# Kernel tuning notes

Hardware: AMD Instinct MI355X
Metric: run time of the kernel (lower is better)

Reference implementation:

```python
import jax, jax.numpy as jnp
import numpy as np

D_MODEL = 1024
N_HEADS = 16
D_FF = 4096
ROPE_THETA = 10000.0


def _rope(x, pos):
    # x: [B, H, S, D], pos: [S]
    D = x.shape[-1]
    inv_freq = ROPE_THETA ** (-jnp.arange(0, D, 2, dtype=jnp.float32) / D)  # [D/2]
    ang = pos.astype(jnp.float32)[:, None] * inv_freq[None, :]              # [S, D/2]
    cos, sin = jnp.cos(ang), jnp.sin(ang)
    x1, x2 = x[..., 0::2], x[..., 1::2]
    r1 = x1 * cos - x2 * sin
    r2 = x1 * sin + x2 * cos
    return jnp.stack([r1, r2], axis=-1).reshape(x.shape)


def _rmsnorm(x, g, eps=1e-5):
    xf = x.astype(jnp.float32)
    rms = jnp.sqrt(jnp.mean(xf * xf, axis=-1, keepdims=True) + eps)
    return (xf / rms * g).astype(x.dtype)


def _block(x, WQ, WK, WV, WO, W1, W2, W3, G1, G2):
    B, S, _ = x.shape
    H, Dh = N_HEADS, D_MODEL // N_HEADS
    pos = jnp.arange(S)

    h = _rmsnorm(x, G1)
    Q = (h @ WQ.T).reshape(B, S, H, Dh).transpose(0, 2, 1, 3)
    K = (h @ WK.T).reshape(B, S, H, Dh).transpose(0, 2, 1, 3)
    V = (h @ WV.T).reshape(B, S, H, Dh).transpose(0, 2, 1, 3)
    Q = _rope(Q, pos)
    K = _rope(K, pos)

    scores = jnp.einsum('bhqd,bhkd->bhqk', Q, K) / jnp.sqrt(jnp.float32(Dh))
    causal = jnp.triu(jnp.ones((S, S), dtype=bool), k=1)
    scores = jnp.where(causal, -jnp.inf, scores.astype(jnp.float32))
    probs = jax.nn.softmax(scores, axis=-1).astype(x.dtype)
    attn = jnp.einsum('bhqk,bhkd->bhqd', probs, V)
    attn = attn.transpose(0, 2, 1, 3).reshape(B, S, D_MODEL)
    x = x + attn @ WO.T

    h = _rmsnorm(x, G2)
    w1x = h @ W1.T
    w3x = h @ W3.T
    ffn = (w1x * jax.nn.sigmoid(w1x) * w3x) @ W2.T
    return x + ffn


def setup_inputs() -> dict:
    key = jax.random.key(0)
    ks = jax.random.split(key, 9)
    sig_a = np.sqrt(2.0 / (D_MODEL + D_MODEL))
    sig_f = np.sqrt(2.0 / (D_FF + D_MODEL))
    x = jax.random.normal(ks[0], (2, 2048, D_MODEL), dtype=jnp.float32)
    def tn(k, shape, sig):
        return jnp.clip(jax.random.normal(k, shape, dtype=jnp.float32) * sig, -3 * sig, 3 * sig)
    return {
        'x': x,
        'WQ': tn(ks[1], (D_MODEL, D_MODEL), sig_a),
        'WK': tn(ks[2], (D_MODEL, D_MODEL), sig_a),
        'WV': tn(ks[3], (D_MODEL, D_MODEL), sig_a),
        'WO': tn(ks[4], (D_MODEL, D_MODEL), sig_a),
        'W1': tn(ks[5], (D_FF, D_MODEL), sig_f),
        'W2': tn(ks[6], (D_MODEL, D_FF), sig_f),
        'W3': tn(ks[7], (D_FF, D_MODEL), sig_f),
        'G1': jnp.ones((D_MODEL,), dtype=jnp.float32),
        'G2': jnp.ones((D_MODEL,), dtype=jnp.float32),
    }


def reference(x, WQ, WK, WV, WO, W1, W2, W3, G1, G2):
    return _block(x, WQ, WK, WV, WO, W1, W2, W3, G1, G2)
```

## Files before the change

### kernel.cpp

```cpp
#include <hip/hip_runtime.h>
#include <stdint.h>

typedef __attribute__((ext_vector_type(8))) short bf16x8;
typedef __attribute__((ext_vector_type(4))) short short4v;
typedef __attribute__((ext_vector_type(4))) float f32x4;

#define MFMA16(a, b, c) __builtin_amdgcn_mfma_f32_16x16x32_bf16((a), (b), (c), 0, 0, 0)

__device__ __forceinline__ float b2f(short s) {
  unsigned u = ((unsigned)(unsigned short)s) << 16;
  return __builtin_bit_cast(float, u);
}
__device__ __forceinline__ short f2b(float f) {
  unsigned u = __builtin_bit_cast(unsigned, f);
  u = (u + 0x7fffu + ((u >> 16) & 1u)) >> 16;
  return (short)u;
}

__device__ __forceinline__ void gl_lds16(const short* g, short* l) {
  __builtin_amdgcn_global_load_lds((const __attribute__((address_space(1))) void*)g,
                                   (__attribute__((address_space(3))) void*)l, 16, 0, 0);
}

__global__ __launch_bounds__(256) void convert_kernel(const float* __restrict__ src,
                                                      short* __restrict__ dst, int n) {
  int i = (blockIdx.x * 256 + threadIdx.x) * 8;
  if (i >= n) return;
  f32x4 a = *(const f32x4*)(src + i);
  f32x4 b = *(const f32x4*)(src + i + 4);
  short4v o0, o1;
#pragma unroll
  for (int j = 0; j < 4; ++j) { o0[j] = f2b(a[j]); o1[j] = f2b(b[j]); }
  *(short4v*)(dst + i) = o0;
  *(short4v*)(dst + i + 4) = o1;
}

__global__ __launch_bounds__(256) void rmsnorm_f32(const float* __restrict__ X,
                                                   const float* __restrict__ G,
                                                   short* __restrict__ O) {
  int row = blockIdx.x;
  int t = threadIdx.x;
  f32x4 v = *(const f32x4*)(X + (size_t)row * 1024 + t * 4);
  float ss = 0.f;
#pragma unroll
  for (int j = 0; j < 4; ++j) ss += v[j] * v[j];
#pragma unroll
  for (int d = 1; d < 64; d <<= 1) ss += __shfl_xor(ss, d, 64);
  __shared__ float red[4];
  if ((t & 63) == 0) red[t >> 6] = ss;
  __syncthreads();
  float tot = red[0] + red[1] + red[2] + red[3];
  float rinv = rsqrtf(tot * (1.0f / 1024.0f) + 1e-5f);
  f32x4 g = *(const f32x4*)(G + t * 4);
  short4v o;
#pragma unroll
  for (int j = 0; j < 4; ++j) o[j] = f2b(v[j] * rinv * g[j]);
  *(short4v*)(O + (size_t)row * 1024 + t * 4) = o;
}

template <int MODE>
__global__ __launch_bounds__(256) void gemm_bt(const short* __restrict__ A,
                                               const short* __restrict__ Bt,
                                               const void* Res, void* C,
                                               void* C1, void* C2,
                                               int M, int N, int K) {
  __shared__ __attribute__((aligned(16))) short Alds[2][128 * 32];
  __shared__ __attribute__((aligned(16))) short Blds[2][128 * 32];
  int tid = threadIdx.x;
  int lane = tid & 63, w = tid >> 6;
  int wr = w >> 1, wc = w & 1;
  int l15 = lane & 15, lg = lane >> 4;
  int m0 = blockIdx.y * 128, n0 = blockIdx.x * 128;
  void* Cw = C;
  int ncol0 = n0;
  int seg = 0;
  if (MODE == 3) {
    seg = n0 >> 10;
    Cw = (seg == 0) ? C : (seg == 1) ? C1 : C2;
    ncol0 = n0 & 1023;
  }
  f32x4 acc[4][4] = {};
  int arow = tid >> 2, acol = (tid & 3) * 8;
  const short* Ap = A + (size_t)(m0 + arow) * K + acol;
  const short* Bp = Bt + (size_t)(n0 + arow) * K + acol;
  int wb = w * 512;
#define STAGE_BT(buf, k0s)                                   \
  {                                                          \
    gl_lds16(Ap + (k0s), &Alds[buf][0] + wb);                \
    gl_lds16(Ap + (size_t)64 * K + (k0s), &Alds[buf][0] + 2048 + wb); \
    gl_lds16(Bp + (k0s), &Blds[buf][0] + wb);                \
    gl_lds16(Bp + (size_t)64 * K + (k0s), &Blds[buf][0] + 2048 + wb); \
  }
  STAGE_BT(0, 0);
  __syncthreads();
  int cur = 0;
  for (int k0 = 0; k0 < K; k0 += 32) {
    if (k0 + 32 < K) STAGE_BT(cur ^ 1, k0 + 32);
    bf16x8 af[4], bfr[4];
#pragma unroll
    for (int i = 0; i < 4; ++i) {
      af[i] = *(const bf16x8*)(&Alds[cur][0] + (wr * 64 + i * 16 + l15) * 32 + lg * 8);
      bfr[i] = *(const bf16x8*)(&Blds[cur][0] + (wc * 64 + i * 16 + l15) * 32 + lg * 8);
    }
#pragma unroll
    for (int mi = 0; mi < 4; ++mi)
#pragma unroll
      for (int ni = 0; ni < 4; ++ni)
        acc[mi][ni] = MFMA16(af[mi], bfr[ni], acc[mi][ni]);
    __syncthreads();
    cur ^= 1;
  }
#undef STAGE_BT
#pragma unroll
  for (int mi = 0; mi < 4; ++mi) {
#pragma unroll
    for (int r = 0; r < 4; ++r) {
      int row = m0 + wr * 64 + mi * 16 + lg * 4 + r;
      size_t base = (size_t)row * N;
#pragma unroll
      for (int ni = 0; ni < 4; ++ni) {
        int col = ncol0 + wc * 64 + ni * 16 + l15;
        float v = acc[mi][ni][r];
        if (MODE == 3 && seg <= 1) {
          int pos = row & 2047;
          int ii = (col & 62) >> 1;
          float invf2 = exp2f(-(float)ii * 0.4152410118f) * 0.15915494309f;
          float rev = (float)pos * invf2;
          rev -= rintf(rev);
          float angr = rev * 6.28318530718f;
          float sn = __sinf(angr), cs = __cosf(angr);
          float partner = __shfl_xor(v, 1, 64);
          float t = partner * sn;
          v = v * cs + (((l15 & 1) == 0) ? -t : t);
        }
        if (MODE == 2) {
          float rr = b2f(((const short*)Res)[base + col]);
          v = rr / (1.f + __expf(-rr)) * v;
          ((short*)Cw)[base + col] = f2b(v);
        } else {
          ((short*)Cw)[base + col] = f2b(v);
        }
      }
    }
  }
}

template <int MODE>
__global__ __launch_bounds__(512) void gemm256(const short* __restrict__ A,
                                               const short* __restrict__ Bt,
                                               const void* Res, void* C,
                                               int M, int N, int K) {
  __shared__ __attribute__((aligned(16))) short Alds[2][256 * 64];
  __shared__ __attribute__((aligned(16))) short Blds[2][256 * 64];
  int tid = threadIdx.x;
  int lane = tid & 63, w = tid >> 6;
  int wr = w >> 2, wc = w & 3;
  int l15 = lane & 15, lg = lane >> 4;
  int wg = blockIdx.x;
  int swz = (wg & 7) * 32 + (wg >> 3);
  int by = swz >> 4, bx = swz & 15;
  int m0 = by * 256, n0 = bx * 256;
  f32x4 acc[8][4] = {};
  int rr = tid >> 3;
  int cs = (tid & 7) ^ (rr & 7);
  const short* Apt = A + (size_t)(m0 + rr) * K + cs * 8;
  const short* Bpt = Bt + (size_t)(n0 + rr) * K + cs * 8;
#define STAGE_256(buf, kt)                                                     \
  {                                                                            \
    int ko = (kt) * 64;                                                        \
    _Pragma("unroll")                                                          \
    for (int j = 0; j < 4; ++j) {                                              \
      gl_lds16(Apt + (size_t)(j * 64) * K + ko, &Alds[buf][0] + j * 4096 + w * 512); \
      gl_lds16(Bpt + (size_t)(j * 64) * K + ko, &Blds[buf][0] + j * 4096 + w * 512); \
    }                                                                          \
  }
  int nt = K >> 6;
  STAGE_256(0, 0);
  __syncthreads();
  int cur = 0;
  for (int kt = 0; kt < nt; ++kt) {
    if (kt + 1 < nt) STAGE_256(cur ^ 1, kt + 1);
#pragma unroll
    for (int kk = 0; kk < 2; ++kk) {
      bf16x8 af[8], bfr[4];
#pragma unroll
      for (int i = 0; i < 8; ++i) {
        int ra = wr * 128 + i * 16 + l15;
        int ua = (kk * 4 + lg) ^ (ra & 7);
        af[i] = *(const bf16x8*)(&Alds[cur][0] + ra * 64 + ua * 8);
      }
#pragma unroll
      for (int n = 0; n < 4; ++n) {
        int rb = wc * 64 + n * 16 + l15;
        int ub = (kk * 4 + lg) ^ (rb & 7);
        bfr[n] = *(const bf16x8*)(&Blds[cur][0] + rb * 64 + ub * 8);
      }
#pragma unroll
      for (int i = 0; i < 8; ++i)
#pragma unroll
        for (int n = 0; n < 4; ++n)
          acc[i][n] = MFMA16(af[i], bfr[n], acc[i][n]);
    }
    __syncthreads();
    cur ^= 1;
  }
#undef STAGE_256
#pragma unroll
  for (int i = 0; i < 8; ++i) {
#pragma unroll
    for (int r = 0; r < 4; ++r) {
      int row = m0 + wr * 128 + i * 16 + lg * 4 + r;
      size_t base = (size_t)row * N;
#pragma unroll
      for (int n = 0; n < 4; ++n) {
        int col = n0 + wc * 64 + n * 16 + l15;
        float v = acc[i][n][r];
        if (MODE == 2) {
          float rr2 = b2f(((const short*)Res)[base + col]);
          v = rr2 / (1.f + __expf(-rr2)) * v;
        }
        ((short*)C)[base + col] = f2b(v);
      }
    }
  }
}

__global__ __launch_bounds__(512) void gemm_wide(const short* __restrict__ A,
                                                 const short* __restrict__ Bt,
                                                 const float* Res, float* C,
                                                 int M, int N, int K) {
  __shared__ __attribute__((aligned(16))) short Alds[4][128 * 64];
  __shared__ __attribute__((aligned(16))) short Blds[4][128 * 64];
  int tid = threadIdx.x;
  int lane = tid & 63, w = tid >> 6;
  int wr = w >> 2, wc = w & 3;
  int l15 = lane & 15, lg = lane >> 4;
  int m0 = blockIdx.y * 128, n0 = blockIdx.x * 128;
  f32x4 acc[4][2] = {};
  int o0 = tid, o1 = 512 + tid;
  int r0 = o0 >> 3, cs0 = (o0 & 7) ^ (r0 & 7);
  int r1 = o1 >> 3, cs1 = (o1 & 7) ^ (r1 & 7);
  const short* Ap0 = A + (size_t)(m0 + r0) * K + cs0 * 8;
  const short* Ap1 = A + (size_t)(m0 + r1) * K + cs1 * 8;
  const short* Bp0 = Bt + (size_t)(n0 + r0) * K + cs0 * 8;
  const short* Bp1 = Bt + (size_t)(n0 + r1) * K + cs1 * 8;
  int wb = w * 512;
#define STG_W(buf, k0s)                                  \
  {                                                      \
    gl_lds16(Ap0 + (k0s), &Alds[buf][0] + wb);           \
    gl_lds16(Ap1 + (k0s), &Alds[buf][0] + 4096 + wb);    \
    gl_lds16(Bp0 + (k0s), &Blds[buf][0] + wb);           \
    gl_lds16(Bp1 + (k0s), &Blds[buf][0] + 4096 + wb);    \
  }
  int nk = K >> 6;
  STG_W(0, 0);
  STG_W(1, 64);
  asm volatile("s_waitcnt vmcnt(4)" ::: "memory");
  __builtin_amdgcn_s_barrier();
  asm volatile("" ::: "memory");
  for (int kt = 0; kt < nk; ++kt) {
    int buf = kt & 3;
    if (kt + 2 < nk) STG_W((kt + 2) & 3, (kt + 2) * 64);
    bf16x8 af[4][2], bfr[2][2];
#pragma unroll
    for (int i = 0; i < 4; ++i) {
      int ra = wr * 64 + i * 16 + l15;
#pragma unroll
      for (int kk = 0; kk < 2; ++kk) {
        int ua = (kk * 4 + lg) ^ (ra & 7);
        af[i][kk] = *(const bf16x8*)(&Alds[buf][0] + ra * 64 + ua * 8);
      }
    }
#pragma unroll
    for (int i = 0; i < 2; ++i) {
      int rb = wc * 32 + i * 16 + l15;
#pragma unroll
      for (int kk = 0; kk < 2; ++kk) {
        int ub = (kk * 4 + lg) ^ (rb & 7);
        bfr[i][kk] = *(const bf16x8*)(&Blds[buf][0] + rb * 64 + ub * 8);
      }
    }
#pragma unroll
    for (int kk = 0; kk < 2; ++kk)
#pragma unroll
      for (int mi = 0; mi < 4; ++mi)
#pragma unroll
        for (int ni = 0; ni < 2; ++ni)
          acc[mi][ni] = MFMA16(af[mi][kk], bfr[ni][kk], acc[mi][ni]);
    if (kt + 2 < nk) {
      asm volatile("s_waitcnt vmcnt(4)" ::: "memory");
    } else {
      asm volatile("s_waitcnt vmcnt(0)" ::: "memory");
    }
    __builtin_amdgcn_s_barrier();
    asm volatile("" ::: "memory");
  }
#undef STG_W
#pragma unroll
  for (int mi = 0; mi < 4; ++mi) {
#pragma unroll
    for (int r = 0; r < 4; ++r) {
      int row = m0 + wr * 64 + mi * 16 + lg * 4 + r;
      size_t base = (size_t)row * N;
#pragma unroll
      for (int ni = 0; ni < 2; ++ni) {
        int col = n0 + wc * 32 + ni * 16 + l15;
        C[base + col] = acc[mi][ni][r] + Res[base + col];
      }
    }
  }
}

__global__ __launch_bounds__(256) void vtranspose(const short* __restrict__ V,
                                                  short* __restrict__ Vt) {
  __shared__ short T[64 * 72];
  int bh = blockIdx.y;
  int s0 = blockIdx.x * 64;
  int t = threadIdx.x;
  int r = t >> 2, cq = t & 3;
  const short* src = V + (size_t)((bh >> 4) * 2048 + s0 + r) * 1024 + (bh & 15) * 64 + cq * 16;
  *(int4*)(T + r * 72 + cq * 16) = *(const int4*)src;
  *(int4*)(T + r * 72 + cq * 16 + 8) = *(const int4*)(src + 8);
  __syncthreads();
  int d = t >> 2, sq = t & 3;
  short* dst = Vt + (size_t)bh * 131072 + (size_t)d * 2048 + s0 + sq * 16;
#pragma unroll
  for (int q = 0; q < 4; ++q) {
    short4v o;
#pragma unroll
    for (int j = 0; j < 4; ++j) o[j] = T[(sq * 16 + q * 4 + j) * 72 + d];
    *(short4v*)(dst + q * 4) = o;
  }
}

__global__ __launch_bounds__(256) void attn6(const short* __restrict__ Q,
                                             const short* __restrict__ K,
                                             const short* __restrict__ Vt,
                                             short* __restrict__ O) {
  __shared__ __attribute__((aligned(16))) short Klds[2][64 * 64];
  __shared__ __attribute__((aligned(16))) short Vlds[2][64 * 64];
  __shared__ __attribute__((aligned(16))) short Ptlds[4][64 * 20];
  int bx = blockIdx.x;
  int bh = bx & 31;
  int qt = 31 - (bx >> 5);
  int tid = threadIdx.x;
  int w = tid >> 6, lane = tid & 63;
  int l15 = lane & 15, lg = lane >> 4;
  int qbase = qt * 64 + w * 16;
  size_t rowbase = (size_t)(bh >> 4) * 2048 * 1024 + (size_t)(bh & 15) * 64;
  const short* vtb = Vt + (size_t)bh * 131072;
  const short* Kb0 = K + rowbase;
  bf16x8 qf[2];
  {
    const short* qp = Q + rowbase + (size_t)(qbase + l15) * 1024 + lg * 8;
    qf[0] = *(const bf16x8*)qp;
    qf[1] = *(const bf16x8*)(qp + 32);
  }
  bf16x8 ones;
#pragma unroll
  for (int j = 0; j < 8; ++j) ones[j] = (short)0x3F80;
  f32x4 oacc[4] = {};
  f32x4 lacc = {};
  int nchunk = qt + 1;
  short* pt = Ptlds[w];
  int i0 = w * 64 + lane;
  int r0 = i0 >> 3, c0 = i0 & 7, cs0 = c0 ^ (r0 & 7);
  int i1 = 256 + i0;
  int r1 = i1 >> 3, c1 = i1 & 7, cs1 = c1 ^ (r1 & 7);
#define STAGE_KV(buf, kt)                                                      \
  {                                                                            \
    int ks = (kt) * 64;                                                        \
    gl_lds16(Kb0 + (size_t)(ks + r0) * 1024 + cs0 * 8, &Klds[buf][0] + i0 * 8);\
    gl_lds16(Kb0 + (size_t)(ks + r1) * 1024 + cs1 * 8, &Klds[buf][0] + i1 * 8);\
    gl_lds16(vtb + (size_t)r0 * 2048 + ks + cs0 * 8, &Vlds[buf][0] + i0 * 8);  \
    gl_lds16(vtb + (size_t)r1 * 2048 + ks + cs1 * 8, &Vlds[buf][0] + i1 * 8);  \
  }
  STAGE_KV(0, 0);
  __syncthreads();
  int cur = 0;
  for (int kt = 0; kt < nchunk; ++kt) {
    if (kt + 1 < nchunk) STAGE_KV(cur ^ 1, kt + 1);
    int kstart = kt * 64;
    f32x4 s[4] = {};
#pragma unroll
    for (int g = 0; g < 4; ++g) {
      int krow = g * 16 + l15;
      bf16x8 k0 = *(const bf16x8*)(&Klds[cur][0] + krow * 64 + ((lg ^ (l15 & 7)) * 8));
      bf16x8 k1 = *(const bf16x8*)(&Klds[cur][0] + krow * 64 + (((4 + lg) ^ (l15 & 7)) * 8));
      s[g] = MFMA16(qf[0], k0, s[g]);
      s[g] = MFMA16(qf[1], k1, s[g]);
    }
#pragma unroll
    for (int g = 0; g < 4; ++g) {
      short4v pk;
#pragma unroll
      for (int r = 0; r < 4; ++r) {
        int qg = qbase + lg * 4 + r;
        int kg = kstart + g * 16 + l15;
        float v = __expf(s[g][r] * 0.125f - 24.f);
        pk[r] = f2b((kg > qg) ? 0.f : v);
      }
      *(short4v*)(pt + (g * 16 + l15) * 20 + lg * 4) = pk;
    }
    bf16x8 pa0, pa1;
#pragma unroll
    for (int j = 0; j < 8; ++j) {
      pa0[j] = pt[(lg * 8 + j) * 20 + l15];
      pa1[j] = pt[(32 + lg * 8 + j) * 20 + l15];
    }
#pragma unroll
    for (int t = 0; t < 4; ++t) {
      int drow = t * 16 + l15;
      bf16x8 vf0 = *(const bf16x8*)(&Vlds[cur][0] + drow * 64 + ((lg ^ (l15 & 7)) * 8));
      bf16x8 vf1 = *(const bf16x8*)(&Vlds[cur][0] + drow * 64 + (((4 + lg) ^ (l15 & 7)) * 8));
      oacc[t] = MFMA16(pa0, vf0, oacc[t]);
      oacc[t] = MFMA16(pa1, vf1, oacc[t]);
    }
    lacc = MFMA16(pa0, ones, lacc);
    lacc = MFMA16(pa1, ones, lacc);
    __syncthreads();
    cur ^= 1;
  }
#undef STAGE_KV
#pragma unroll
  for (int t = 0; t < 4; ++t) {
#pragma unroll
    for (int r = 0; r < 4; ++r) {
      int row = qbase + lg * 4 + r;
      float denom = fmaxf(lacc[r], 1e-30f);
      O[rowbase + (size_t)row * 1024 + t * 16 + l15] = f2b(oacc[t][r] / denom);
    }
  }
}

extern "C" void kernel_launch(void* const* d_in, const int* in_sizes, int n_in,
                              void* d_out, int out_size, void* d_ws, size_t ws_size,
                              hipStream_t stream) {
  const float* xf = (const float*)d_in[0];
  const float* G1f = (const float*)d_in[8];
  const float* G2f = (const float*)d_in[9];
  char* ws = (char*)d_ws;
  const size_t MB = 1048576;
  short* Wslot = (short*)(ws);
  short* WOb   = (short*)(ws);
  short* Wcat  = (short*)(ws + 8 * MB);
  short* Vt    = (short*)(ws + 8 * MB);
  short* h     = (short*)(ws + 16 * MB);
  short* Qb    = (short*)(ws + 24 * MB);
  short* Kb    = (short*)(ws + 32 * MB);
  short* Vb    = (short*)(ws + 40 * MB);
  short* att   = (short*)(ws + 48 * MB);
  short* w1x   = Qb;
  float* x1f   = (float*)d_out;
  float* outf  = (float*)d_out;

  dim3 blk(256);
  convert_kernel<<<512, blk, 0, stream>>>((const float*)d_in[1], Wcat, 1048576);
  convert_kernel<<<512, blk, 0, stream>>>((const float*)d_in[2], Wcat + 1048576, 1048576);
  convert_kernel<<<512, blk, 0, stream>>>((const float*)d_in[3], Wcat + 2097152, 1048576);
  convert_kernel<<<512, blk, 0, stream>>>((const float*)d_in[4], WOb, 1048576);

  rmsnorm_f32<<<4096, blk, 0, stream>>>(xf, G1f, h);
  dim3 gqkv(24, 32);
  gemm_bt<3><<<gqkv, blk, 0, stream>>>(h, Wcat, nullptr, Qb, Kb, Vb, 4096, 1024, 1024);
  dim3 gvt(32, 32);
  vtranspose<<<gvt, blk, 0, stream>>>(Vb, Vt);
  attn6<<<1024, blk, 0, stream>>>(Qb, Kb, Vt, att);
  dim3 g1(8, 32);
  gemm_wide<<<g1, dim3(512), 0, stream>>>(att, WOb, xf, x1f, 4096, 1024, 1024);
  rmsnorm_f32<<<4096, blk, 0, stream>>>(x1f, G2f, h);
  convert_kernel<<<2048, blk, 0, stream>>>((const float*)d_in[5], Wslot, 4194304);
  gemm256<0><<<256, dim3(512), 0, stream>>>(h, Wslot, nullptr, w1x, 4096, 4096, 1024);
  convert_kernel<<<2048, blk, 0, stream>>>((const float*)d_in[7], Wslot, 4194304);
  gemm256<2><<<256, dim3(512), 0, stream>>>(h, Wslot, w1x, w1x, 4096, 4096, 1024);
  convert_kernel<<<2048, blk, 0, stream>>>((const float*)d_in[6], Wslot, 4194304);
  gemm_wide<<<g1, dim3(512), 0, stream>>>(w1x, Wslot, x1f, outf, 4096, 1024, 4096);
}
```

Baseline: 331.7 us.

## Restructure 256x256 GEMM mainloop into four-phase interleaved load/MFMA schedule

Rewrites the gemm256 main loop so each k-tile is split into four phases. Each phase loads a quarter of the A/B fragments from LDS, issues one half-tile of the next global->LDS stage, and runs a quarter of the MFMAs between explicit s_barrier/s_waitcnt points. s_setprio is raised around the MFMA blocks. The goal is to overlap global and LDS traffic with matrix math and to cut register pressure from holding full fragment sets, at the cost of many more barriers per iteration and hand-managed waitcnt ordering.

```diff
diff --git a/kernel.cpp b/kernel.cpp
--- a/kernel.cpp
+++ b/kernel.cpp
@@ -150,8 +150,8 @@
                                                const short* __restrict__ Bt,
                                                const void* Res, void* C,
                                                int M, int N, int K) {
-  __shared__ __attribute__((aligned(16))) short Alds[2][256 * 64];
-  __shared__ __attribute__((aligned(16))) short Blds[2][256 * 64];
+  __shared__ __attribute__((aligned(16))) short Al[2][2][128 * 64];
+  __shared__ __attribute__((aligned(16))) short Bl[2][2][128 * 64];
   int tid = threadIdx.x;
   int lane = tid & 63, w = tid >> 6;
   int wr = w >> 2, wc = w & 3;
@@ -161,50 +161,100 @@
   int by = swz >> 4, bx = swz & 15;
   int m0 = by * 256, n0 = bx * 256;
   f32x4 acc[8][4] = {};
-  int rr = tid >> 3;
-  int cs = (tid & 7) ^ (rr & 7);
-  const short* Apt = A + (size_t)(m0 + rr) * K + cs * 8;
-  const short* Bpt = Bt + (size_t)(n0 + rr) * K + cs * 8;
-#define STAGE_256(buf, kt)                                                     \
-  {                                                                            \
-    int ko = (kt) * 64;                                                        \
-    _Pragma("unroll")                                                          \
-    for (int j = 0; j < 4; ++j) {                                              \
-      gl_lds16(Apt + (size_t)(j * 64) * K + ko, &Alds[buf][0] + j * 4096 + w * 512); \
-      gl_lds16(Bpt + (size_t)(j * 64) * K + ko, &Blds[buf][0] + j * 4096 + w * 512); \
-    }                                                                          \
-  }
-  int nt = K >> 6;
-  STAGE_256(0, 0);
-  __syncthreads();
-  int cur = 0;
-  for (int kt = 0; kt < nt; ++kt) {
-    if (kt + 1 < nt) STAGE_256(cur ^ 1, kt + 1);
-#pragma unroll
-    for (int kk = 0; kk < 2; ++kk) {
-      bf16x8 af[8], bfr[4];
-#pragma unroll
-      for (int i = 0; i < 8; ++i) {
-        int ra = wr * 128 + i * 16 + l15;
-        int ua = (kk * 4 + lg) ^ (ra & 7);
-        af[i] = *(const bf16x8*)(&Alds[cur][0] + ra * 64 + ua * 8);
-      }
-#pragma unroll
-      for (int n = 0; n < 4; ++n) {
-        int rb = wc * 64 + n * 16 + l15;
-        int ub = (kk * 4 + lg) ^ (rb & 7);
-        bfr[n] = *(const bf16x8*)(&Blds[cur][0] + rb * 64 + ub * 8);
-      }
-#pragma unroll
-      for (int i = 0; i < 8; ++i)
-#pragma unroll
-        for (int n = 0; n < 4; ++n)
-          acc[i][n] = MFMA16(af[i], bfr[n], acc[i][n]);
-    }
-    __syncthreads();
-    cur ^= 1;
-  }
-#undef STAGE_256
+  int r0 = tid >> 3, c0 = tid & 7;
+  int cs0 = c0 ^ (r0 & 7);
+  int r1 = 64 + r0;
+  int cs1 = c0 ^ (r1 & 7);
+  int wso = w * 512;
+
+#define STG_HALF(dsth, srcp, x0, hh, ktile)                                        \
+  {                                                                                \
+    gl_lds16((srcp) + (size_t)((x0) + (hh) * 128 + r0) * K + (ktile) * 64 + cs0 * 8, \
+             (dsth) + wso);                                                        \
+    gl_lds16((srcp) + (size_t)((x0) + (hh) * 128 + r1) * K + (ktile) * 64 + cs1 * 8, \
+             (dsth) + 4096 + wso);                                                 \
+  }
+#define DSR_A(qb)                                                                  \
+  _Pragma("unroll") for (int i = 0; i < 4; ++i) {                                  \
+    int rl = ((qb) + i) * 16 + l15;                                                \
+    _Pragma("unroll") for (int kk = 0; kk < 2; ++kk)                               \
+      af[i][kk] = *(const bf16x8*)(Asl + rl * 64 + (((kk * 4 + lg) ^ (l15 & 7)) * 8)); \
+  }
+#define DSR_B(nb)                                                                  \
+  _Pragma("unroll") for (int n = 0; n < 2; ++n) {                                  \
+    int rl = (wc & 1) * 64 + ((nb) + n) * 16 + l15;                                \
+    _Pragma("unroll") for (int kk = 0; kk < 2; ++kk)                               \
+      bfv[n][kk] = *(const bf16x8*)(Bsl + rl * 64 + (((kk * 4 + lg) ^ (l15 & 7)) * 8)); \
+  }
+#define MM(ib, nb)                                                                 \
+  _Pragma("unroll") for (int kk = 0; kk < 2; ++kk)                                 \
+  _Pragma("unroll") for (int i = 0; i < 4; ++i)                                    \
+  _Pragma("unroll") for (int n = 0; n < 2; ++n)                                    \
+    acc[(ib) + i][(nb) + n] = MFMA16(af[i][kk], bfv[n][kk], acc[(ib) + i][(nb) + n]);
+#define BAR asm volatile("s_barrier" ::: "memory")
+#define LGK0                                        \
+  asm volatile("s_waitcnt lgkmcnt(0)" ::: "memory"); \
+  __builtin_amdgcn_sched_barrier(0)
+
+  STG_HALF(&Al[0][0][0], A, m0, 0, 0);
+  STG_HALF(&Al[0][1][0], A, m0, 1, 0);
+  STG_HALF(&Bl[0][0][0], Bt, n0, 0, 0);
+  STG_HALF(&Bl[0][1][0], Bt, n0, 1, 0);
+  asm volatile("s_waitcnt vmcnt(0)" ::: "memory");
+  BAR;
+
+  int nkt = K >> 6;
+  for (int kt = 0; kt < nkt; ++kt) {
+    int s = kt & 1;
+    const short* Asl = &Al[s][wr][0];
+    const short* Bsl = &Bl[s][wc >> 1][0];
+    short* Ad0 = &Al[s ^ 1][0][0];
+    short* Ad1 = &Al[s ^ 1][1][0];
+    short* Bd0 = &Bl[s ^ 1][0][0];
+    short* Bd1 = &Bl[s ^ 1][1][0];
+    bool st = (kt + 1 < nkt);
+    bf16x8 af[4][2], bfv[2][2];
+    DSR_A(0);
+    DSR_B(0);
+    if (st) STG_HALF(Ad0, A, m0, 0, kt + 1);
+    BAR;
+    LGK0;
+    __builtin_amdgcn_s_setprio(1);
+    MM(0, 0);
+    __builtin_amdgcn_s_setprio(0);
+    BAR;
+    DSR_B(2);
+    if (st) STG_HALF(Ad1, A, m0, 1, kt + 1);
+    BAR;
+    LGK0;
+    __builtin_amdgcn_s_setprio(1);
+    MM(0, 2);
+    __builtin_amdgcn_s_setprio(0);
+    BAR;
+    DSR_A(4);
+    if (st) STG_HALF(Bd0, Bt, n0, 0, kt + 1);
+    BAR;
+    LGK0;
+    __builtin_amdgcn_s_setprio(1);
+    MM(4, 2);
+    __builtin_amdgcn_s_setprio(0);
+    BAR;
+    DSR_B(0);
+    if (st) STG_HALF(Bd1, Bt, n0, 1, kt + 1);
+    BAR;
+    LGK0;
+    __builtin_amdgcn_s_setprio(1);
+    MM(4, 0);
+    __builtin_amdgcn_s_setprio(0);
+    if (st) asm volatile("s_waitcnt vmcnt(0)" ::: "memory");
+    BAR;
+  }
+#undef STG_HALF
+#undef DSR_A
+#undef DSR_B
+#undef MM
+#undef BAR
+#undef LGK0
 #pragma unroll
   for (int i = 0; i < 8; ++i) {
 #pragma unroll
```

Result: no change. 331.3 us (-0.1%).

## Fuse W1 and W3 FFN GEMMs into one kernel and add XCD-aware tile mapping

Applied to the files above, without the earlier changes.

Replaces the two separate gate/up GEMM launches with one kernel that runs the W1 K-loop, stashes the result as bf16 in registers, then runs the W3 K-loop and applies SiLU-gating in the epilogue. This drops the intermediate w1x write and re-read and the extra launch, and lets W3 conversion go to its own buffer. It also remaps gemm_wide blocks so consecutive row tiles land on the same XCD for better L2 reuse. The register stash adds pressure (64 more VGPRs) on an already heavy 8x4 accumulator kernel, which may cause spills.

```diff
diff --git a/kernel.cpp b/kernel.cpp
--- a/kernel.cpp
+++ b/kernel.cpp
@@ -133,23 +133,17 @@
           float t = partner * sn;
           v = v * cs + (((l15 & 1) == 0) ? -t : t);
         }
-        if (MODE == 2) {
-          float rr = b2f(((const short*)Res)[base + col]);
-          v = rr / (1.f + __expf(-rr)) * v;
-          ((short*)Cw)[base + col] = f2b(v);
-        } else {
-          ((short*)Cw)[base + col] = f2b(v);
-        }
-      }
-    }
-  }
-}
-
-template <int MODE>
-__global__ __launch_bounds__(512) void gemm256(const short* __restrict__ A,
-                                               const short* __restrict__ Bt,
-                                               const void* Res, void* C,
-                                               int M, int N, int K) {
+        ((short*)Cw)[base + col] = f2b(v);
+      }
+    }
+  }
+}
+
+__global__ __launch_bounds__(512) void gemm256_fused(const short* __restrict__ A,
+                                                     const short* __restrict__ B1,
+                                                     const short* __restrict__ B3,
+                                                     short* __restrict__ C,
+                                                     int M, int N, int K) {
   __shared__ __attribute__((aligned(16))) short Alds[2][256 * 64];
   __shared__ __attribute__((aligned(16))) short Blds[2][256 * 64];
   int tid = threadIdx.x;
@@ -160,51 +154,73 @@
   int swz = (wg & 7) * 32 + (wg >> 3);
   int by = swz >> 4, bx = swz & 15;
   int m0 = by * 256, n0 = bx * 256;
-  f32x4 acc[8][4] = {};
   int rr = tid >> 3;
   int cs = (tid & 7) ^ (rr & 7);
   const short* Apt = A + (size_t)(m0 + rr) * K + cs * 8;
-  const short* Bpt = Bt + (size_t)(n0 + rr) * K + cs * 8;
-#define STAGE_256(buf, kt)                                                     \
-  {                                                                            \
-    int ko = (kt) * 64;                                                        \
-    _Pragma("unroll")                                                          \
-    for (int j = 0; j < 4; ++j) {                                              \
-      gl_lds16(Apt + (size_t)(j * 64) * K + ko, &Alds[buf][0] + j * 4096 + w * 512); \
-      gl_lds16(Bpt + (size_t)(j * 64) * K + ko, &Blds[buf][0] + j * 4096 + w * 512); \
-    }                                                                          \
-  }
+  const short* Bpt1 = B1 + (size_t)(n0 + rr) * K + cs * 8;
+  const short* Bpt3 = B3 + (size_t)(n0 + rr) * K + cs * 8;
   int nt = K >> 6;
-  STAGE_256(0, 0);
-  __syncthreads();
-  int cur = 0;
-  for (int kt = 0; kt < nt; ++kt) {
-    if (kt + 1 < nt) STAGE_256(cur ^ 1, kt + 1);
-#pragma unroll
-    for (int kk = 0; kk < 2; ++kk) {
-      bf16x8 af[8], bfr[4];
-#pragma unroll
-      for (int i = 0; i < 8; ++i) {
-        int ra = wr * 128 + i * 16 + l15;
-        int ua = (kk * 4 + lg) ^ (ra & 7);
-        af[i] = *(const bf16x8*)(&Alds[cur][0] + ra * 64 + ua * 8);
-      }
-#pragma unroll
-      for (int n = 0; n < 4; ++n) {
-        int rb = wc * 64 + n * 16 + l15;
-        int ub = (kk * 4 + lg) ^ (rb & 7);
-        bfr[n] = *(const bf16x8*)(&Blds[cur][0] + rb * 64 + ub * 8);
-      }
-#pragma unroll
-      for (int i = 0; i < 8; ++i)
-#pragma unroll
-        for (int n = 0; n < 4; ++n)
-          acc[i][n] = MFMA16(af[i], bfr[n], acc[i][n]);
-    }
-    __syncthreads();
-    cur ^= 1;
-  }
-#undef STAGE_256
+  f32x4 acc[8][4];
+  short4v stash[8][4];
+#define STAGE_A(buf, kt)                                                             \
+  {                                                                                  \
+    int ko = (kt) * 64;                                                              \
+    _Pragma("unroll") for (int j = 0; j < 4; ++j)                                    \
+        gl_lds16(Apt + (size_t)(j * 64) * K + ko, &Alds[buf][0] + j * 4096 + w * 512); \
+  }
+#define STAGE_B(buf, kt, Bp)                                                         \
+  {                                                                                  \
+    int ko = (kt) * 64;                                                              \
+    _Pragma("unroll") for (int j = 0; j < 4; ++j)                                    \
+        gl_lds16((Bp) + (size_t)(j * 64) * K + ko, &Blds[buf][0] + j * 4096 + w * 512); \
+  }
+#define KLOOP(Bp)                                                                    \
+  {                                                                                  \
+    STAGE_A(0, 0);                                                                   \
+    STAGE_B(0, 0, Bp);                                                               \
+    __syncthreads();                                                                 \
+    int cur = 0;                                                                     \
+    for (int kt = 0; kt < nt; ++kt) {                                                \
+      if (kt + 1 < nt) { STAGE_A(cur ^ 1, kt + 1); STAGE_B(cur ^ 1, kt + 1, Bp); }   \
+      _Pragma("unroll") for (int kk = 0; kk < 2; ++kk) {                             \
+        bf16x8 af[8], bfr[4];                                                        \
+        _Pragma("unroll") for (int i = 0; i < 8; ++i) {                              \
+          int ra = wr * 128 + i * 16 + l15;                                          \
+          int ua = (kk * 4 + lg) ^ (ra & 7);                                         \
+          af[i] = *(const bf16x8*)(&Alds[cur][0] + ra * 64 + ua * 8);                \
+        }                                                                            \
+        _Pragma("unroll") for (int n = 0; n < 4; ++n) {                              \
+          int rb = wc * 64 + n * 16 + l15;                                           \
+          int ub = (kk * 4 + lg) ^ (rb & 7);                                         \
+          bfr[n] = *(const bf16x8*)(&Blds[cur][0] + rb * 64 + ub * 8);               \
+        }                                                                            \
+        _Pragma("unroll") for (int i = 0; i < 8; ++i)                                \
+        _Pragma("unroll") for (int n = 0; n < 4; ++n)                                \
+            acc[i][n] = MFMA16(af[i], bfr[n], acc[i][n]);                            \
+      }                                                                              \
+      __syncthreads();                                                               \
+      cur ^= 1;                                                                      \
+    }                                                                                \
+  }
+#pragma unroll
+  for (int i = 0; i < 8; ++i)
+#pragma unroll
+    for (int n = 0; n < 4; ++n) acc[i][n] = (f32x4){0.f, 0.f, 0.f, 0.f};
+  KLOOP(Bpt1);
+#pragma unroll
+  for (int i = 0; i < 8; ++i)
+#pragma unroll
+    for (int n = 0; n < 4; ++n)
+#pragma unroll
+      for (int r = 0; r < 4; ++r) stash[i][n][r] = f2b(acc[i][n][r]);
+#pragma unroll
+  for (int i = 0; i < 8; ++i)
+#pragma unroll
+    for (int n = 0; n < 4; ++n) acc[i][n] = (f32x4){0.f, 0.f, 0.f, 0.f};
+  KLOOP(Bpt3);
+#undef KLOOP
+#undef STAGE_A
+#undef STAGE_B
 #pragma unroll
   for (int i = 0; i < 8; ++i) {
 #pragma unroll
@@ -214,12 +230,9 @@
 #pragma unroll
       for (int n = 0; n < 4; ++n) {
         int col = n0 + wc * 64 + n * 16 + l15;
-        float v = acc[i][n][r];
-        if (MODE == 2) {
-          float rr2 = b2f(((const short*)Res)[base + col]);
-          v = rr2 / (1.f + __expf(-rr2)) * v;
-        }
-        ((short*)C)[base + col] = f2b(v);
+        float w1v = b2f(stash[i][n][r]);
+        float v = w1v / (1.f + __expf(-w1v)) * acc[i][n][r];
+        C[base + col] = f2b(v);
       }
     }
   }
@@ -235,7 +248,12 @@
   int lane = tid & 63, w = tid >> 6;
   int wr = w >> 2, wc = w & 3;
   int l15 = lane & 15, lg = lane >> 4;
-  int m0 = blockIdx.y * 128, n0 = blockIdx.x * 128;
+  int lin = blockIdx.y * gridDim.x + blockIdx.x;
+  int nx = gridDim.x;
+  int xcd = lin & 7, idx = lin >> 3;
+  int mpX = (gridDim.y >> 3);
+  int m0 = (xcd * mpX + idx / nx) * 128;
+  int n0 = (idx % nx) * 128;
   f32x4 acc[4][2] = {};
   int o0 = tid, o1 = 512 + tid;
   int r0 = o0 >> 3, cs0 = (o0 & 7) ^ (r0 & 7);
@@ -450,6 +468,7 @@
   short* Kb    = (short*)(ws + 32 * MB);
   short* Vb    = (short*)(ws + 40 * MB);
   short* att   = (short*)(ws + 48 * MB);
+  short* W3b   = (short*)(ws + 56 * MB);
   short* w1x   = Qb;
   float* x1f   = (float*)d_out;
   float* outf  = (float*)d_out;
@@ -470,9 +489,8 @@
   gemm_wide<<<g1, dim3(512), 0, stream>>>(att, WOb, xf, x1f, 4096, 1024, 1024);
   rmsnorm_f32<<<4096, blk, 0, stream>>>(x1f, G2f, h);
   convert_kernel<<<2048, blk, 0, stream>>>((const float*)d_in[5], Wslot, 4194304);
-  gemm256<0><<<256, dim3(512), 0, stream>>>(h, Wslot, nullptr, w1x, 4096, 4096, 1024);
-  convert_kernel<<<2048, blk, 0, stream>>>((const float*)d_in[7], Wslot, 4194304);
-  gemm256<2><<<256, dim3(512), 0, stream>>>(h, Wslot, w1x, w1x, 4096, 4096, 1024);
+  convert_kernel<<<2048, blk, 0, stream>>>((const float*)d_in[7], W3b, 4194304);
+  gemm256_fused<<<256, dim3(512), 0, stream>>>(h, Wslot, W3b, w1x, 4096, 4096, 1024);
   convert_kernel<<<2048, blk, 0, stream>>>((const float*)d_in[6], Wslot, 4194304);
   gemm_wide<<<g1, dim3(512), 0, stream>>>(w1x, Wslot, x1f, outf, 4096, 1024, 4096);
 }
```

Measured after the change: 303.1 us, median of 2. 1.09x faster.
